# Performance work log

Hardware: AMD Instinct MI355X
Metric: run time of the kernel (lower is better)

Reference implementation:

```python
import jax, jax.numpy as jnp
import numpy as np

H = 4          # num_heads (= num_kv_heads, num_kv_groups = 1)
DK = 256       # head_k_dim
DV = 256       # head_v_dim
M = 256        # num_slots
GATE_NORM = 16.0
EPS = 1e-5


def _rmsnorm(x, w):
    var = jnp.mean(jnp.square(x), axis=-1, keepdims=True)
    return x * jax.lax.rsqrt(var + EPS) * w


def _swish(x):
    return x * jax.nn.sigmoid(x)


def setup_inputs() -> dict:
    key = jax.random.key(0)
    ks = jax.random.split(key, 8)
    B, T, D = 4, 2048, 1024
    scale = 2 ** (-2.5) * (2.0 / (D + D)) ** 0.5 * (3.0 ** 0.5) * 2  # ~xavier*gain magnitude
    return {
        "hidden_states": jax.random.normal(ks[0], (B, T, D), jnp.float32),
        "norm_weight": jnp.ones((D,), jnp.float32),
        "w_q": jax.random.normal(ks[1], (D, D), jnp.float32) * scale,
        "w_k": jax.random.normal(ks[2], (D, D), jnp.float32) * scale,
        "w_v": jax.random.normal(ks[3], (D, D), jnp.float32) * scale,
        "w_f": jax.random.normal(ks[4], (H * M, D), jnp.float32) * scale,
        "gnorm_weight": jnp.ones((D,), jnp.float32),
        "w_o": jax.random.normal(ks[5], (D, D), jnp.float32) * scale,
    }


def _gsa_scan(q, k, v, s, g):
    # all inputs time-major: q [T,B,H,DK], k [T,B,H,DK], v [T,B,H,DV],
    # s [T,B,H,M] (slot write strength), g [T,B,H,M] (log forget gate)
    B, Hh = q.shape[1], q.shape[2]
    Hk0 = jnp.zeros((B, Hh, DK, M), q.dtype)
    Hv0 = jnp.zeros((B, Hh, M, DV), q.dtype)

    def step(carry, xs):
        Hk, Hv = carry
        qt, kt, vt, st, gt = xs
        lam = jnp.exp(gt)                                       # [B,H,M]
        # pass 1: linear attn over slots (gate on value/slot dim)
        Hk = Hk * lam[:, :, None, :] + kt[..., :, None] * st[..., None, :]
        z = jnp.einsum('bhk,bhkm->bhm', qt, Hk)                 # slot logits
        p = jax.nn.softmax(z, axis=-1)                          # slot read weights
        # pass 2: linear attn from slots to values (gate on key/slot dim)
        Hv = Hv * lam[..., :, None] + st[..., :, None] * vt[..., None, :]
        ot = jnp.einsum('bhm,bhmv->bhv', p, Hv)
        return (Hk, Hv), ot

    _, o = jax.lax.scan(step, (Hk0, Hv0), (q, k, v, s, g))
    return o  # [T,B,H,DV]


def reference(hidden_states, norm_weight, w_q, w_k, w_v, w_f, gnorm_weight, w_o):
    B, T, D = hidden_states.shape
    h = _rmsnorm(hidden_states, norm_weight)                    # norm_first
    q = _swish(h @ w_q.T).reshape(B, T, H, DK)                  # swish feature map
    k = _swish(h @ w_k.T).reshape(B, T, H, DK)
    v = _swish(h @ w_v.T).reshape(B, T, H, DV)
    f = jax.nn.log_sigmoid(h @ w_f.T).reshape(B, T, H, M) / GATE_NORM
    s = 1.0 - jnp.exp(f)
    tm = lambda x: jnp.transpose(x, (1, 0, 2, 3))               # [B,T,H,*] -> [T,B,H,*]
    o = _gsa_scan(tm(q), tm(k), tm(v), tm(s), tm(f))            # [T,B,H,DV]
    o = jnp.transpose(o, (1, 0, 2, 3)).reshape(B, T, H * DV)
    # use_norm & no output gate: swish -> RMSNorm -> o_proj
    o = _swish(o)
    o = _rmsnorm(o, gnorm_weight)
    return o @ w_o.T
```

## Files before the change

### kernel.cpp

```cpp
#include <hip/hip_runtime.h>
#include <hip/hip_bf16.h>

typedef unsigned short u16;
typedef unsigned int u32;

using bf16x8 = __bf16 __attribute__((ext_vector_type(8)));
using s16x8  = short  __attribute__((ext_vector_type(8)));
using f32x4  = float  __attribute__((ext_vector_type(4)));

#define DEV static __device__ __forceinline__

constexpr int T_ = 2048, D_ = 1024;
constexpr int C_ = 64, NC_ = 32;
constexpr float EPS_ = 1e-5f;

DEV float bf2f(u16 u) { return __uint_as_float(((u32)u) << 16); }
DEV u16 f2bf(float f) {
  u32 u = __float_as_uint(f);
  return (u16)((u + 0x7fffu + ((u >> 16) & 1u)) >> 16);
}
DEV float swishf(float x) { return x / (1.f + __expf(-x)); }
DEV f32x4 zero4() { f32x4 z = {0.f, 0.f, 0.f, 0.f}; return z; }

DEV bf16x8 ld8(const u16* p, int ld, int r0, int k0, int lane) {
  return *(const bf16x8*)(p + (size_t)(r0 + (lane & 15)) * ld +
                          (size_t)(k0 + ((lane >> 4) << 3)));
}
DEV f32x4 MFMA(bf16x8 a, bf16x8 b, f32x4 c) {
  return __builtin_amdgcn_mfma_f32_16x16x32_bf16(a, b, c, 0, 0, 0);
}
DEV void gld_lds16(const void* g, void* l) {
  __builtin_amdgcn_global_load_lds(
      (const __attribute__((address_space(1))) unsigned int*)g,
      (__attribute__((address_space(3))) unsigned int*)l, 16, 0, 0);
}

__global__ __launch_bounds__(256) void k_cvt5(
    const float* __restrict__ s0, const float* __restrict__ s1,
    const float* __restrict__ s2, const float* __restrict__ s3,
    const float* __restrict__ s4, u16* __restrict__ d0, u16* __restrict__ d1,
    u16* __restrict__ d2, u16* __restrict__ d3, u16* __restrict__ d4) {
  const int wsel = blockIdx.x >> 10;
  const float* s = (wsel == 0) ? s0 : (wsel == 1) ? s1 : (wsel == 2) ? s2
                   : (wsel == 3) ? s3 : s4;
  u16* d = (wsel == 0) ? d0 : (wsel == 1) ? d1 : (wsel == 2) ? d2
           : (wsel == 3) ? d3 : d4;
  const int i = (blockIdx.x & 1023) * 256 + threadIdx.x;
  float4 v = ((const float4*)s)[i];
  uint2 o;
  o.x = (u32)f2bf(v.x) | ((u32)f2bf(v.y) << 16);
  o.y = (u32)f2bf(v.z) | ((u32)f2bf(v.w) << 16);
  ((uint2*)d)[i] = o;
}

__global__ __launch_bounds__(256) void k_rmsnorm(const float* __restrict__ x,
                                                 const float* __restrict__ w,
                                                 u16* __restrict__ h) {
  const int row = blockIdx.x, tid = threadIdx.x;
  float4 v = ((const float4*)(x + (size_t)row * D_))[tid];
  float ss = v.x * v.x + v.y * v.y + v.z * v.z + v.w * v.w;
#pragma unroll
  for (int d = 32; d >= 1; d >>= 1) ss += __shfl_xor(ss, d, 64);
  __shared__ float red[4];
  if ((tid & 63) == 0) red[tid >> 6] = ss;
  __syncthreads();
  float rs = rsqrtf((red[0] + red[1] + red[2] + red[3]) * (1.f / D_) + EPS_);
  float4 wv = ((const float4*)w)[tid];
  uint2 o;
  o.x = (u32)f2bf(v.x * rs * wv.x) | ((u32)f2bf(v.y * rs * wv.y) << 16);
  o.y = (u32)f2bf(v.z * rs * wv.z) | ((u32)f2bf(v.w * rs * wv.w) << 16);
  *(uint2*)(h + (size_t)row * D_ + tid * 4) = o;
}

__global__ __launch_bounds__(256) void k_swishnorm(const u16* __restrict__ x,
                                                   const float* __restrict__ w,
                                                   u16* __restrict__ o) {
  const int row = blockIdx.x, tid = threadIdx.x;
  uint2 pk = *(const uint2*)(x + (size_t)row * D_ + tid * 4);
  float v0 = swishf(bf2f((u16)(pk.x & 0xffff))), v1 = swishf(bf2f((u16)(pk.x >> 16)));
  float v2 = swishf(bf2f((u16)(pk.y & 0xffff))), v3 = swishf(bf2f((u16)(pk.y >> 16)));
  float ss = v0 * v0 + v1 * v1 + v2 * v2 + v3 * v3;
#pragma unroll
  for (int d = 32; d >= 1; d >>= 1) ss += __shfl_xor(ss, d, 64);
  __shared__ float red[4];
  if ((tid & 63) == 0) red[tid >> 6] = ss;
  __syncthreads();
  float rs = rsqrtf((red[0] + red[1] + red[2] + red[3]) * (1.f / D_) + EPS_);
  float4 wv = ((const float4*)w)[tid];
  uint2 ov;
  ov.x = (u32)f2bf(v0 * rs * wv.x) | ((u32)f2bf(v1 * rs * wv.y) << 16);
  ov.y = (u32)f2bf(v2 * rs * wv.z) | ((u32)f2bf(v3 * rs * wv.w) << 16);
  *(uint2*)(o + (size_t)row * D_ + tid * 4) = ov;
}

__global__ __launch_bounds__(256) void k_gemm4f(
    const u16* __restrict__ A, const u16* __restrict__ w0,
    const u16* __restrict__ w1, const u16* __restrict__ w2,
    const u16* __restrict__ w3, u16* __restrict__ oq, u16* __restrict__ okk,
    u16* __restrict__ ov, float* __restrict__ og) {
  __shared__ __align__(16) u16 As[128 * 32];
  __shared__ __align__(16) u16 Bs[128 * 32];
  const int m0 = blockIdx.x * 128;
  const int wsel = blockIdx.y >> 3;
  const int n0 = (blockIdx.y & 7) * 128;
  const u16* W = (wsel == 0) ? w0 : (wsel == 1) ? w1 : (wsel == 2) ? w2 : w3;
  const int tid = threadIdx.x, lane = tid & 63, wvi = tid >> 6;
  const int wr = wvi >> 1, wc = wvi & 1;
  f32x4 acc[4][4];
#pragma unroll
  for (int i = 0; i < 4; i++)
#pragma unroll
    for (int j = 0; j < 4; j++) acc[i][j] = zero4();
  const int srow = tid >> 2, scb = (tid & 3) * 8;
  const u16* Ag = A + (size_t)(m0 + srow) * 1024 + scb;
  const u16* Wg = W + (size_t)(n0 + srow) * 1024 + scb;
  u16* AsW = As + (wvi * 16) * 32;
  u16* BsW = Bs + (wvi * 16) * 32;
  for (int kk = 0; kk < 1024; kk += 32) {
    gld_lds16(Ag + kk, AsW);
    gld_lds16(Ag + kk + 64 * 1024, AsW + 64 * 32);
    gld_lds16(Wg + kk, BsW);
    gld_lds16(Wg + kk + 64 * 1024, BsW + 64 * 32);
    __syncthreads();
    bf16x8 af[4], bfr[4];
#pragma unroll
    for (int i = 0; i < 4; i++) af[i] = ld8(As, 32, wr * 64 + 16 * i, 0, lane);
#pragma unroll
    for (int j = 0; j < 4; j++) bfr[j] = ld8(Bs, 32, wc * 64 + 16 * j, 0, lane);
#pragma unroll
    for (int i = 0; i < 4; i++)
#pragma unroll
      for (int j = 0; j < 4; j++) acc[i][j] = MFMA(af[i], bfr[j], acc[i][j]);
    __syncthreads();
  }
  const int q4 = lane >> 4, c15 = lane & 15;
  u16* obf = (wsel == 0) ? oq : (wsel == 1) ? okk : ov;
#pragma unroll
  for (int i = 0; i < 4; i++)
#pragma unroll
    for (int j = 0; j < 4; j++)
#pragma unroll
      for (int r = 0; r < 4; r++) {
        int grow = m0 + wr * 64 + 16 * i + 4 * q4 + r;
        int gcol = n0 + wc * 64 + 16 * j + c15;
        size_t idx = (size_t)grow * 1024 + gcol;
        float val = acc[i][j][r];
        if (wsel < 3) {
          obf[idx] = f2bf(swishf(val));
        } else {
          float g = (val >= 0.f) ? -log1pf(__expf(-val))
                                 : (val - log1pf(__expf(val)));
          og[idx] = g * (1.0f / 16.0f);
        }
      }
}

__global__ __launch_bounds__(256) void k_gemmO(const u16* __restrict__ A,
                                               const u16* __restrict__ W,
                                               float* __restrict__ ofin) {
  __shared__ __align__(16) u16 As[128 * 32];
  __shared__ __align__(16) u16 Bs[128 * 32];
  const int m0 = blockIdx.x * 128, n0 = blockIdx.y * 128;
  const int tid = threadIdx.x, lane = tid & 63, wvi = tid >> 6;
  const int wr = wvi >> 1, wc = wvi & 1;
  f32x4 acc[4][4];
#pragma unroll
  for (int i = 0; i < 4; i++)
#pragma unroll
    for (int j = 0; j < 4; j++) acc[i][j] = zero4();
  const int srow = tid >> 2, scb = (tid & 3) * 8;
  const u16* Ag = A + (size_t)(m0 + srow) * 1024 + scb;
  const u16* Wg = W + (size_t)(n0 + srow) * 1024 + scb;
  u16* AsW = As + (wvi * 16) * 32;
  u16* BsW = Bs + (wvi * 16) * 32;
  for (int kk = 0; kk < 1024; kk += 32) {
    gld_lds16(Ag + kk, AsW);
    gld_lds16(Ag + kk + 64 * 1024, AsW + 64 * 32);
    gld_lds16(Wg + kk, BsW);
    gld_lds16(Wg + kk + 64 * 1024, BsW + 64 * 32);
    __syncthreads();
    bf16x8 af[4], bfr[4];
#pragma unroll
    for (int i = 0; i < 4; i++) af[i] = ld8(As, 32, wr * 64 + 16 * i, 0, lane);
#pragma unroll
    for (int j = 0; j < 4; j++) bfr[j] = ld8(Bs, 32, wc * 64 + 16 * j, 0, lane);
#pragma unroll
    for (int i = 0; i < 4; i++)
#pragma unroll
      for (int j = 0; j < 4; j++) acc[i][j] = MFMA(af[i], bfr[j], acc[i][j]);
    __syncthreads();
  }
  const int q4 = lane >> 4, c15 = lane & 15;
#pragma unroll
  for (int i = 0; i < 4; i++)
#pragma unroll
    for (int j = 0; j < 4; j++)
#pragma unroll
      for (int r = 0; r < 4; r++) {
        int grow = m0 + wr * 64 + 16 * i + 4 * q4 + r;
        int gcol = n0 + wc * 64 + 16 * j + c15;
        ofin[(size_t)grow * 1024 + gcol] = acc[i][j][r];
      }
}

__global__ __launch_bounds__(256) void k_gates(float* __restrict__ g_inout,
                                               u16* __restrict__ U_t,
                                               float* __restrict__ Lam) {
  const int c = blockIdx.x, p = blockIdx.y, tid = threadIdx.x;
  const int b = p >> 2, hh = p & 3;
  const int R0 = b * T_ + c * C_, hb = hh * 256;
  float ga = 0.f, ea = 1.f;
  short ubuf[C_];
#pragma unroll
  for (int t = 0; t < C_; t++) {
    size_t gi = (size_t)(R0 + t) * D_ + hb + tid;
    float gv = g_inout[gi];
    ga += gv;
    ea = __expf(ga);
    ubuf[t] = (short)f2bf((1.f - __expf(gv)) * __expf(-ga));
    g_inout[gi] = ea;
  }
  Lam[((size_t)p * NC_ + c) * 256 + tid] = ea;
  u16* up = U_t + ((size_t)p * NC_ + c) * (256 * C_) + (size_t)tid * C_;
#pragma unroll
  for (int i = 0; i < 8; i++) {
    s16x8 w;
#pragma unroll
    for (int j = 0; j < 8; j++) w[j] = ubuf[i * 8 + j];
    *(s16x8*)(up + i * 8) = w;
  }
}

__global__ __launch_bounds__(256) void k_intra(
    const u16* __restrict__ kg, const u16* __restrict__ vg,
    const u16* __restrict__ U_t, const float* __restrict__ Lam,
    u16* __restrict__ Sk, u16* __restrict__ Sv) {
  __shared__ __align__(16) u16 KV[256 * 72];
  __shared__ float LamH[256];
  const int c = blockIdx.x, p = blockIdx.y;
  const int b = p >> 2, hh = p & 3;
  const int R0 = b * T_ + c * C_, hb = hh * 256;
  const int tid = threadIdx.x, lane = tid & 63, wvi = tid >> 6;
  const int q4 = lane >> 4, c15 = lane & 15;
  const size_t chunk = (size_t)p * NC_ + c;
  const u16* Uc = U_t + chunk * (256 * C_);
  const size_t scBase = chunk * (256 * 256);

  LamH[tid] = Lam[chunk * 256 + tid];
  for (int t = 0; t < C_; t++)
    KV[tid * 72 + t] = kg[(size_t)(R0 + t) * D_ + hb + tid];
  __syncthreads();

  for (int cb = 0; cb < 4; cb++) {
    f32x4 acc[4][4];
#pragma unroll
    for (int i = 0; i < 4; i++)
#pragma unroll
      for (int j = 0; j < 4; j++) acc[i][j] = zero4();
#pragma unroll
    for (int ks = 0; ks < 2; ks++) {
      bf16x8 af[4], bfr[4];
#pragma unroll
      for (int i = 0; i < 4; i++) af[i] = ld8(Uc, C_, 64 * wvi + 16 * i, 32 * ks, lane);
#pragma unroll
      for (int j = 0; j < 4; j++) bfr[j] = ld8(KV, 72, 64 * cb + 16 * j, 32 * ks, lane);
#pragma unroll
      for (int i = 0; i < 4; i++)
#pragma unroll
        for (int j = 0; j < 4; j++) acc[i][j] = MFMA(af[i], bfr[j], acc[i][j]);
    }
#pragma unroll
    for (int i = 0; i < 4; i++)
#pragma unroll
      for (int j = 0; j < 4; j++)
#pragma unroll
        for (int r = 0; r < 4; r++) {
          int ml = 64 * wvi + 16 * i + 4 * q4 + r;
          int dd = 64 * cb + 16 * j + c15;
          Sk[scBase + (size_t)ml * 256 + dd] = f2bf(acc[i][j][r] * LamH[ml]);
        }
  }
  __syncthreads();

  for (int t = 0; t < C_; t++)
    KV[tid * 72 + t] = vg[(size_t)(R0 + t) * D_ + hb + tid];
  __syncthreads();

  for (int cb = 0; cb < 4; cb++) {
    f32x4 acc[4][4];
#pragma unroll
    for (int i = 0; i < 4; i++)
#pragma unroll
      for (int j = 0; j < 4; j++) acc[i][j] = zero4();
#pragma unroll
    for (int ks = 0; ks < 2; ks++) {
      bf16x8 af[4], bfr[4];
#pragma unroll
      for (int i = 0; i < 4; i++) af[i] = ld8(KV, 72, 64 * wvi + 16 * i, 32 * ks, lane);
#pragma unroll
      for (int j = 0; j < 4; j++) bfr[j] = ld8(Uc, C_, 64 * cb + 16 * j, 32 * ks, lane);
#pragma unroll
      for (int i = 0; i < 4; i++)
#pragma unroll
        for (int j = 0; j < 4; j++) acc[i][j] = MFMA(af[i], bfr[j], acc[i][j]);
    }
#pragma unroll
    for (int i = 0; i < 4; i++)
#pragma unroll
      for (int j = 0; j < 4; j++)
#pragma unroll
        for (int r = 0; r < 4; r++) {
          int vv = 64 * wvi + 16 * i + 4 * q4 + r;
          int ml = 64 * cb + 16 * j + c15;
          Sv[scBase + (size_t)vv * 256 + ml] = f2bf(acc[i][j][r] * LamH[ml]);
        }
  }
}

__global__ __launch_bounds__(256) void k_scan(u16* __restrict__ Sk,
                                              u16* __restrict__ Sv,
                                              const float* __restrict__ Lam) {
  const int gid = blockIdx.x * 256 + threadIdx.x;
  const int st = gid >> 17;
  const int w = gid & 131071;
  const int p = w >> 13;
  const int r = (w >> 5) & 255;
  const int c0 = (w & 31) * 8;
  u16* S = st ? Sv : Sk;
  const size_t base = (size_t)p * NC_ * 65536 + (size_t)r * 256 + c0;
  const float* Lp = Lam + (size_t)p * NC_ * 256;
  float acc[8] = {0, 0, 0, 0, 0, 0, 0, 0};
  for (int c = 0; c < NC_; c++) {
    s16x8 in = *(const s16x8*)(S + base + (size_t)c * 65536);
    s16x8 ov;
#pragma unroll
    for (int j = 0; j < 8; j++) ov[j] = (short)f2bf(acc[j]);
    *(s16x8*)(S + base + (size_t)c * 65536) = ov;
    if (st == 0) {
      float lam = Lp[c * 256 + r];
#pragma unroll
      for (int j = 0; j < 8; j++) acc[j] = acc[j] * lam + bf2f((u16)in[j]);
    } else {
#pragma unroll
      for (int j = 0; j < 8; j++) {
        float lam = Lp[c * 256 + c0 + j];
        acc[j] = acc[j] * lam + bf2f((u16)in[j]);
      }
    }
  }
}

__global__ __launch_bounds__(256) void k_out(
    const u16* __restrict__ qg, const u16* __restrict__ kg,
    const u16* __restrict__ vg, const u16* __restrict__ U_t,
    const float* __restrict__ Eg, const u16* __restrict__ Sk,
    const u16* __restrict__ Sv, u16* __restrict__ orw) {
  __shared__ __align__(16) char lds[61440];
  u16* As = (u16*)lds;
  u16* Pt = (u16*)(lds + 9216);
  u16* UnH = (u16*)(lds + 43008);
  u16* VxH = (u16*)(lds + 43008);

  const int c = blockIdx.x, p = blockIdx.y;
  const int b = p >> 2, hh = p & 3;
  const int R0 = b * T_ + c * C_, hb = hh * 256;
  const int tid = threadIdx.x, lane = tid & 63, wvi = tid >> 6;
  const int q4 = lane >> 4, c15 = lane & 15;
  const u16* qbase = qg + (size_t)R0 * D_ + hb;
  const u16* kbase = kg + (size_t)R0 * D_ + hb;
  const float* Ebase = Eg + (size_t)R0 * D_ + hb;
  const size_t chunk = (size_t)p * NC_ + c;
  const u16* SkC = Sk + chunk * 65536;
  const u16* SvC = Sv + chunk * 65536;
  const u16* Uc = U_t + chunk * (256 * C_);

  {
    f32x4 acc[4];
#pragma unroll
    for (int n = 0; n < 4; n++) acc[n] = zero4();
#pragma unroll
    for (int ks = 0; ks < 8; ks++) {
      bf16x8 af = ld8(qbase, D_, 16 * wvi, 32 * ks, lane);
#pragma unroll
      for (int n = 0; n < 4; n++)
        acc[n] = MFMA(af, ld8(kbase, D_, 16 * n, 32 * ks, lane), acc[n]);
    }
#pragma unroll
    for (int n = 0; n < 4; n++)
#pragma unroll
      for (int r = 0; r < 4; r++) {
        int t = 16 * wvi + 4 * q4 + r, tau = 16 * n + c15;
        As[t * 72 + tau] = f2bf(tau <= t ? acc[n][r] : 0.f);
      }
  }
  __syncthreads();

  f32x4 zac[16], eRg[16];
#pragma unroll
  for (int mh = 0; mh < 2; mh++) {
#pragma unroll
    for (int n = 0; n < 8; n++) zac[mh * 8 + n] = zero4();
#pragma unroll
    for (int ks = 0; ks < 2; ks++) {
      bf16x8 af = ld8(As, 72, 16 * wvi, 32 * ks, lane);
#pragma unroll
      for (int n = 0; n < 8; n++)
        zac[mh * 8 + n] = MFMA(af, ld8(Uc, C_, mh * 128 + 16 * n, 32 * ks, lane),
                               zac[mh * 8 + n]);
    }
#pragma unroll
    for (int ks = 0; ks < 8; ks++) {
      bf16x8 af = ld8(qbase, D_, 16 * wvi, 32 * ks, lane);
#pragma unroll
      for (int n = 0; n < 8; n++)
        zac[mh * 8 + n] = MFMA(
            af, ld8(SkC + (size_t)mh * 128 * 256, 256, 16 * n, 32 * ks, lane),
            zac[mh * 8 + n]);
    }
#pragma unroll
    for (int n = 0; n < 8; n++)
#pragma unroll
      for (int r = 0; r < 4; r++) {
        int t = 16 * wvi + 4 * q4 + r;
        float e = Ebase[(size_t)t * D_ + mh * 128 + 16 * n + c15];
        eRg[mh * 8 + n][r] = e;
        zac[mh * 8 + n][r] *= e;
      }
  }

#pragma unroll
  for (int r = 0; r < 4; r++) {
    float mx = -3.0e38f;
#pragma unroll
    for (int i = 0; i < 16; i++) mx = fmaxf(mx, zac[i][r]);
    mx = fmaxf(mx, __shfl_xor(mx, 1, 64));
    mx = fmaxf(mx, __shfl_xor(mx, 2, 64));
    mx = fmaxf(mx, __shfl_xor(mx, 4, 64));
    mx = fmaxf(mx, __shfl_xor(mx, 8, 64));
    float sm = 0.f;
#pragma unroll
    for (int i = 0; i < 16; i++) {
      float e = __expf(zac[i][r] - mx);
      zac[i][r] = e;
      sm += e;
    }
    sm += __shfl_xor(sm, 1, 64);
    sm += __shfl_xor(sm, 2, 64);
    sm += __shfl_xor(sm, 4, 64);
    sm += __shfl_xor(sm, 8, 64);
    float inv = 1.f / sm;
#pragma unroll
    for (int i = 0; i < 16; i++) zac[i][r] *= inv * eRg[i][r];
  }
#pragma unroll
  for (int i = 0; i < 16; i++)
#pragma unroll
    for (int r = 0; r < 4; r++) {
      int t = 16 * wvi + 4 * q4 + r;
      int m = (i >> 3) * 128 + 16 * (i & 7) + c15;
      Pt[t * 264 + m] = f2bf(zac[i][r]);
    }
  __syncthreads();

  {
    f32x4 wac[4];
#pragma unroll
    for (int n = 0; n < 4; n++) wac[n] = zero4();
    for (int mh = 0; mh < 2; mh++) {
      {
        int mloc = tid >> 1, th = tid & 1;
        const u16* ur = Uc + (size_t)(mh * 128 + mloc) * C_ + th * 32;
#pragma unroll
        for (int tt = 0; tt < 4; tt++) {
          s16x8 v = *(const s16x8*)(ur + tt * 8);
#pragma unroll
          for (int j = 0; j < 8; j++)
            UnH[(th * 32 + tt * 8 + j) * 132 + mloc] = (u16)v[j];
        }
      }
      __syncthreads();
#pragma unroll
      for (int ks = 0; ks < 4; ks++) {
        bf16x8 af = ld8(Pt, 264, 16 * wvi, mh * 128 + 32 * ks, lane);
#pragma unroll
        for (int n = 0; n < 4; n++)
          wac[n] = MFMA(af, ld8(UnH, 132, 16 * n, 32 * ks, lane), wac[n]);
      }
      __syncthreads();
    }
#pragma unroll
    for (int n = 0; n < 4; n++)
#pragma unroll
      for (int r = 0; r < 4; r++) {
        int t = 16 * wvi + 4 * q4 + r, tau = 16 * n + c15;
        As[t * 72 + tau] = f2bf(tau <= t ? wac[n][r] : 0.f);
      }
  }
  __syncthreads();

  for (int vh = 0; vh < 2; vh++) {
    {
      int vloc = tid >> 1, th = tid & 1;
#pragma unroll 4
      for (int tt = 0; tt < 32; tt++) {
        int t = th * 32 + tt;
        VxH[vloc * 72 + t] = vg[(size_t)(R0 + t) * D_ + hb + vh * 128 + vloc];
      }
    }
    __syncthreads();
    f32x4 oac[8];
#pragma unroll
    for (int n = 0; n < 8; n++) oac[n] = zero4();
#pragma unroll
    for (int ks = 0; ks < 8; ks++) {
      bf16x8 af = ld8(Pt, 264, 16 * wvi, 32 * ks, lane);
#pragma unroll
      for (int n = 0; n < 8; n++)
        oac[n] = MFMA(af, ld8(SvC + (size_t)vh * 128 * 256, 256, 16 * n, 32 * ks, lane), oac[n]);
    }
#pragma unroll
    for (int ks = 0; ks < 2; ks++) {
      bf16x8 af = ld8(As, 72, 16 * wvi, 32 * ks, lane);
#pragma unroll
      for (int n = 0; n < 8; n++)
        oac[n] = MFMA(af, ld8(VxH, 72, 16 * n, 32 * ks, lane), oac[n]);
    }
#pragma unroll
    for (int n = 0; n < 8; n++)
#pragma unroll
      for (int r = 0; r < 4; r++) {
        int t = 16 * wvi + 4 * q4 + r;
        int vc = vh * 128 + 16 * n + c15;
        orw[(size_t)(R0 + t) * D_ + hb + vc] = f2bf(oac[n][r]);
      }
    __syncthreads();
  }
}

extern "C" void kernel_launch(void* const* d_in, const int* in_sizes, int n_in,
                              void* d_out, int out_size, void* d_ws, size_t ws_size,
                              hipStream_t stream) {
  (void)in_sizes; (void)n_in; (void)out_size; (void)ws_size;
  const float* x   = (const float*)d_in[0];
  const float* nw  = (const float*)d_in[1];
  const float* wq  = (const float*)d_in[2];
  const float* wk  = (const float*)d_in[3];
  const float* wvp = (const float*)d_in[4];
  const float* wf  = (const float*)d_in[5];
  const float* gw  = (const float*)d_in[6];
  const float* wo  = (const float*)d_in[7];
  float* out = (float*)d_out;
  char* ws = (char*)d_ws;
  const size_t MB = 1024ull * 1024ull;
  u16*   hbuf = (u16*)(ws);
  u16*   qb   = (u16*)(ws + 16 * MB);
  u16*   kb   = (u16*)(ws + 32 * MB);
  u16*   vb   = (u16*)(ws + 48 * MB);
  float* gb   = (float*)(ws + 64 * MB);
  u16*   SkB  = (u16*)(ws + 96 * MB);
  u16*   SvB  = (u16*)(ws + 160 * MB);
  float* Lam  = (float*)(ws + 224 * MB);
  u16*   orw  = (u16*)(ws + 226 * MB);
  u16*   wqb  = (u16*)(ws + 242 * MB);
  u16*   wkb  = (u16*)(ws + 244 * MB);
  u16*   wvb  = (u16*)(ws + 246 * MB);
  u16*   wfb  = (u16*)(ws + 248 * MB);
  u16*   wob  = (u16*)(ws + 250 * MB);
  u16*   U_t  = hbuf;

  k_cvt5<<<dim3(5120), dim3(256), 0, stream>>>(wq, wk, wvp, wf, wo,
                                               wqb, wkb, wvb, wfb, wob);
  k_rmsnorm<<<dim3(8192), dim3(256), 0, stream>>>(x, nw, hbuf);
  k_gemm4f<<<dim3(64, 32), dim3(256), 0, stream>>>(
      hbuf, wqb, wkb, wvb, wfb, qb, kb, vb, gb);
  k_gates<<<dim3(NC_, 16), dim3(256), 0, stream>>>(gb, U_t, Lam);
  k_intra<<<dim3(NC_, 16), dim3(256), 0, stream>>>(kb, vb, U_t, Lam, SkB, SvB);
  k_scan<<<dim3(1024), dim3(256), 0, stream>>>(SkB, SvB, Lam);
  k_out<<<dim3(NC_, 16), dim3(256), 0, stream>>>(qb, kb, vb, U_t, gb, SkB, SvB, orw);
  k_swishnorm<<<dim3(8192), dim3(256), 0, stream>>>(orw, gw, hbuf);
  k_gemmO<<<dim3(64, 8), dim3(256), 0, stream>>>(hbuf, wob, out);
}
```

Before: 531.9 us.

## Rewrite QKVF projection GEMM with 256x256 tiles and a 4-slot LDS ring pipeline

Replaces the 128x128 single-buffered QKV/F projection GEMM with a 256x256 tile, 512-thread kernel. It uses a four-slot LDS ring with XOR-swizzled layout and K-step 64, and interleaves global-to-LDS prefetch with MFMA phases under explicit barriers, vmcnt waits and setprio. The aim is to hide global load latency, cut LDS bank conflicts and raise arithmetic intensity per block. In exchange it uses 128KB of LDS and one block per CU, with only 512 blocks, which risks lower occupancy and tail effects.

```diff
diff --git a/kernel.cpp b/kernel.cpp
--- a/kernel.cpp
+++ b/kernel.cpp
@@ -93,58 +93,129 @@
   *(uint2*)(o + (size_t)row * D_ + tid * 4) = ov;
 }
 
-__global__ __launch_bounds__(256) void k_gemm4f(
+#define SB0() __builtin_amdgcn_sched_barrier(0)
+#define BAR_PRE() do { SB0(); __builtin_amdgcn_s_barrier(); \
+  asm volatile("s_waitcnt lgkmcnt(0)" ::: "memory"); SB0(); } while (0)
+#define BAR_POST() do { SB0(); __builtin_amdgcn_s_barrier(); SB0(); } while (0)
+#define BAR_POSTV(n) do { SB0(); \
+  asm volatile("s_waitcnt vmcnt(" #n ")" ::: "memory"); \
+  __builtin_amdgcn_s_barrier(); SB0(); } while (0)
+
+__global__ __launch_bounds__(512, 1) void k_gemm4(
     const u16* __restrict__ A, const u16* __restrict__ w0,
     const u16* __restrict__ w1, const u16* __restrict__ w2,
     const u16* __restrict__ w3, u16* __restrict__ oq, u16* __restrict__ okk,
     u16* __restrict__ ov, float* __restrict__ og) {
-  __shared__ __align__(16) u16 As[128 * 32];
-  __shared__ __align__(16) u16 Bs[128 * 32];
-  const int m0 = blockIdx.x * 128;
-  const int wsel = blockIdx.y >> 3;
-  const int n0 = (blockIdx.y & 7) * 128;
-  const u16* W = (wsel == 0) ? w0 : (wsel == 1) ? w1 : (wsel == 2) ? w2 : w3;
+  __shared__ __align__(16) u16 Aring[4][128 * 64];
+  __shared__ __align__(16) u16 Bring[4][128 * 64];
+  const int by = blockIdx.y;
+  const int wsel = by >> 2;
+  const int nb = (by & 3) * 256;
+  const int m0 = blockIdx.x * 256;
+  const u16* Wb = (wsel == 0) ? w0 : (wsel == 1) ? w1 : (wsel == 2) ? w2 : w3;
   const int tid = threadIdx.x, lane = tid & 63, wvi = tid >> 6;
-  const int wr = wvi >> 1, wc = wvi & 1;
-  f32x4 acc[4][4];
-#pragma unroll
-  for (int i = 0; i < 4; i++)
+  const int wm = wvi >> 2, wn = wvi & 3;
+
+  f32x4 acc[8][4];
+#pragma unroll
+  for (int i = 0; i < 8; i++)
 #pragma unroll
     for (int j = 0; j < 4; j++) acc[i][j] = zero4();
-  const int srow = tid >> 2, scb = (tid & 3) * 8;
-  const u16* Ag = A + (size_t)(m0 + srow) * 1024 + scb;
-  const u16* Wg = W + (size_t)(n0 + srow) * 1024 + scb;
-  u16* AsW = As + (wvi * 16) * 32;
-  u16* BsW = Bs + (wvi * 16) * 32;
-  for (int kk = 0; kk < 1024; kk += 32) {
-    gld_lds16(Ag + kk, AsW);
-    gld_lds16(Ag + kk + 64 * 1024, AsW + 64 * 32);
-    gld_lds16(Wg + kk, BsW);
-    gld_lds16(Wg + kk + 64 * 1024, BsW + 64 * 32);
-    __syncthreads();
-    bf16x8 af[4], bfr[4];
-#pragma unroll
-    for (int i = 0; i < 4; i++) af[i] = ld8(As, 32, wr * 64 + 16 * i, 0, lane);
-#pragma unroll
-    for (int j = 0; j < 4; j++) bfr[j] = ld8(Bs, 32, wc * 64 + 16 * j, 0, lane);
-#pragma unroll
-    for (int i = 0; i < 4; i++)
-#pragma unroll
-      for (int j = 0; j < 4; j++) acc[i][j] = MFMA(af[i], bfr[j], acc[i][j]);
-    __syncthreads();
-  }
+
+  const int l8 = lane >> 3, l7 = lane & 7;
+  const int srow = wvi * 16 + l8;
+  const int scol = ((l7 ^ l8) << 4);
+  const char* AgB = (const char*)A + (size_t)(m0 + srow) * 2048 + scol;
+  const char* BgB = (const char*)Wb + (size_t)(nb + srow) * 2048 + scol;
+  const int ldsW = wvi * 2048;
+
+  const int rbyte = (lane & 15) * 128;
+  const int x0 = (((lane >> 4)) ^ (lane & 7)) * 16;
+  const int x1 = (((lane >> 4) + 4) ^ (lane & 7)) * 16;
+
+  bf16x8 afr[4][2], bfr0[2][2], bfr1[2][2];
+
+#define STAGE_A(slot, h, kt) do { \
+    const char* g_ = AgB + (size_t)(h) * (128 * 2048) + (kt) * 128; \
+    gld_lds16(g_, (char*)Aring[slot] + ldsW); \
+    gld_lds16(g_ + 8 * 2048, (char*)Aring[slot] + ldsW + 1024); \
+  } while (0)
+#define STAGE_B(slot, h, kt) do { \
+    const char* g_ = BgB + (size_t)(h) * (128 * 2048) + (kt) * 128; \
+    gld_lds16(g_, (char*)Bring[slot] + ldsW); \
+    gld_lds16(g_ + 8 * 2048, (char*)Bring[slot] + ldsW + 1024); \
+  } while (0)
+#define RD_A(par, mh) do { \
+    const char* b_ = (const char*)Aring[(par) * 2 + wm] + (mh) * 64 * 128; \
+    _Pragma("unroll") for (int a_ = 0; a_ < 4; a_++) { \
+      afr[a_][0] = *(const bf16x8*)(b_ + a_ * 16 * 128 + rbyte + x0); \
+      afr[a_][1] = *(const bf16x8*)(b_ + a_ * 16 * 128 + rbyte + x1); \
+    } } while (0)
+#define RD_B(par, nh, dst) do { \
+    const char* b_ = (const char*)Bring[(par) * 2 + (wn >> 1)] + \
+                     ((wn & 1) * 64 + (nh) * 32) * 128; \
+    _Pragma("unroll") for (int c_ = 0; c_ < 2; c_++) { \
+      dst[c_][0] = *(const bf16x8*)(b_ + c_ * 16 * 128 + rbyte + x0); \
+      dst[c_][1] = *(const bf16x8*)(b_ + c_ * 16 * 128 + rbyte + x1); \
+    } } while (0)
+#define MM(mh, nh, bf) do { \
+    __builtin_amdgcn_s_setprio(1); \
+    _Pragma("unroll") for (int a_ = 0; a_ < 4; a_++) \
+      _Pragma("unroll") for (int c_ = 0; c_ < 2; c_++) { \
+        acc[(mh) * 4 + a_][(nh) * 2 + c_] = \
+            MFMA(afr[a_][0], bf[c_][0], acc[(mh) * 4 + a_][(nh) * 2 + c_]); \
+        acc[(mh) * 4 + a_][(nh) * 2 + c_] = \
+            MFMA(afr[a_][1], bf[c_][1], acc[(mh) * 4 + a_][(nh) * 2 + c_]); \
+      } \
+    __builtin_amdgcn_s_setprio(0); \
+  } while (0)
+
+  STAGE_A(0, 0, 0); STAGE_A(1, 1, 0);
+  STAGE_B(0, 0, 0); STAGE_B(1, 1, 0);
+  STAGE_B(2, 0, 1); STAGE_B(3, 1, 1);
+  BAR_POSTV(4);
+
+  for (int it = 0; it < 8; ++it) {
+    const int k1 = 2 * it + 1, k2 = 2 * it + 2, k3 = 2 * it + 3;
+    const bool more = (it < 7);
+    RD_A(0, 0); RD_B(0, 0, bfr0);
+    STAGE_A(2, 0, k1);
+    BAR_PRE(); MM(0, 0, bfr0); BAR_POST();
+    RD_B(0, 1, bfr1);
+    STAGE_A(3, 1, k1);
+    BAR_PRE(); MM(0, 1, bfr1); BAR_POST();
+    RD_A(0, 1);
+    if (more) STAGE_B(0, 0, k2);
+    BAR_PRE(); MM(1, 0, bfr0); BAR_POST();
+    if (more) STAGE_B(1, 1, k2);
+    BAR_PRE(); MM(1, 1, bfr1);
+    if (more) { BAR_POSTV(4); } else { BAR_POSTV(0); }
+    RD_A(1, 0); RD_B(1, 0, bfr0);
+    if (more) STAGE_A(0, 0, k2);
+    BAR_PRE(); MM(0, 0, bfr0); BAR_POST();
+    RD_B(1, 1, bfr1);
+    if (more) STAGE_A(1, 1, k2);
+    BAR_PRE(); MM(0, 1, bfr1); BAR_POST();
+    RD_A(1, 1);
+    if (more) STAGE_B(2, 0, k3);
+    BAR_PRE(); MM(1, 0, bfr0); BAR_POST();
+    if (more) STAGE_B(3, 1, k3);
+    BAR_PRE(); MM(1, 1, bfr1);
+    if (more) { BAR_POSTV(4); } else { BAR_POST(); }
+  }
+
   const int q4 = lane >> 4, c15 = lane & 15;
   u16* obf = (wsel == 0) ? oq : (wsel == 1) ? okk : ov;
 #pragma unroll
-  for (int i = 0; i < 4; i++)
-#pragma unroll
-    for (int j = 0; j < 4; j++)
+  for (int mi = 0; mi < 8; mi++)
+#pragma unroll
+    for (int nj = 0; nj < 4; nj++)
 #pragma unroll
       for (int r = 0; r < 4; r++) {
-        int grow = m0 + wr * 64 + 16 * i + 4 * q4 + r;
-        int gcol = n0 + wc * 64 + 16 * j + c15;
+        int grow = m0 + wm * 128 + mi * 16 + 4 * q4 + r;
+        int gcol = nb + wn * 64 + nj * 16 + c15;
         size_t idx = (size_t)grow * 1024 + gcol;
-        float val = acc[i][j][r];
+        float val = acc[mi][nj][r];
         if (wsel < 3) {
           obf[idx] = f2bf(swishf(val));
         } else {
@@ -153,6 +224,11 @@
           og[idx] = g * (1.0f / 16.0f);
         }
       }
+#undef STAGE_A
+#undef STAGE_B
+#undef RD_A
+#undef RD_B
+#undef MM
 }
 
 __global__ __launch_bounds__(256) void k_gemmO(const u16* __restrict__ A,
@@ -571,7 +647,7 @@
   k_cvt5<<<dim3(5120), dim3(256), 0, stream>>>(wq, wk, wvp, wf, wo,
                                                wqb, wkb, wvb, wfb, wob);
   k_rmsnorm<<<dim3(8192), dim3(256), 0, stream>>>(x, nw, hbuf);
-  k_gemm4f<<<dim3(64, 32), dim3(256), 0, stream>>>(
+  k_gemm4<<<dim3(32, 16), dim3(512), 0, stream>>>(
       hbuf, wqb, wkb, wvb, wfb, qb, kb, vb, gb);
   k_gates<<<dim3(NC_, 16), dim3(256), 0, stream>>>(gb, U_t, Lam);
   k_intra<<<dim3(NC_, 16), dim3(256), 0, stream>>>(kb, vb, U_t, Lam, SkB, SvB);
```

New measurement: 661.4 us. 1.24x slower.
